# Optimization experiments

Measured on AMD Instinct MI355X. Metric: run time of the kernel, lower is better.

The kernel has to match this reference:

```python
import jax, jax.numpy as jnp
import numpy as np

B, C, L = 32, 256, 4096

def _bn(x, g, b, m, v, eps=1e-5):
    # x: [B, C, L]; eval-mode batchnorm with running stats
    inv = jax.lax.rsqrt(v + eps)
    return (x - m[None, :, None]) * (inv * g)[None, :, None] + b[None, :, None]

def _ln(x, g, b, eps=1e-6):
    # layernorm over last dim
    mu = jnp.mean(x, axis=-1, keepdims=True)
    var = jnp.mean(jnp.square(x - mu), axis=-1, keepdims=True)
    return (x - mu) * jax.lax.rsqrt(var + eps) * g + b

def _conv1d(x, w, stride=1):
    # x: [B, Cin, L], w: [Cout, Cin, K]
    return jax.lax.conv_general_dilated(
        x, w, window_strides=(stride,), padding=[(1, 1)],
        dimension_numbers=('NCW', 'OIW', 'NCW'))

def _dct2_matrix(n, dtype):
    # scipy.fftpack.dct type-II, norm=None: y[k] = 2*sum_n x[n]*cos(pi*k*(2n+1)/(2N))
    k = jnp.arange(n, dtype=dtype)[:, None]
    m = jnp.arange(n, dtype=dtype)[None, :]
    return 2.0 * jnp.cos(jnp.pi * k * (2.0 * m + 1.0) / (2.0 * n))


def setup_inputs() -> dict:
    key = jax.random.key(0)
    ks = jax.random.split(key, 12)
    s_conv = 1.0 / np.sqrt(C * 3)
    s_fc1 = 1.0 / np.sqrt(C)
    s_fc2 = 1.0 / np.sqrt(2 * C)
    return {
        'x': jax.random.normal(ks[0], (B, C, L), jnp.float32),
        'conv1_w': jax.random.normal(ks[1], (C, C, 3), jnp.float32) * s_conv,
        'bn1_g': jnp.ones((C,), jnp.float32),
        'bn1_b': jnp.zeros((C,), jnp.float32),
        'bn1_m': jax.random.normal(ks[2], (C,), jnp.float32) * 0.1,
        'bn1_v': jax.random.uniform(ks[3], (C,), jnp.float32, 0.5, 1.5),
        'conv2_w': jax.random.normal(ks[4], (C, C, 3), jnp.float32) * s_conv,
        'bn2_g': jnp.ones((C,), jnp.float32),
        'bn2_b': jnp.zeros((C,), jnp.float32),
        'bn2_m': jax.random.normal(ks[5], (C,), jnp.float32) * 0.1,
        'bn2_v': jax.random.uniform(ks[6], (C,), jnp.float32, 0.5, 1.5),
        'fc1_w': jax.random.normal(ks[7], (2 * C, C), jnp.float32) * s_fc1,
        'fc2_w': jax.random.normal(ks[8], (C, 2 * C), jnp.float32) * s_fc2,
        'ln_g': jnp.ones((C,), jnp.float32),
        'ln_b': jnp.zeros((C,), jnp.float32),
    }


def reference(x, conv1_w, bn1_g, bn1_b, bn1_m, bn1_v,
              conv2_w, bn2_g, bn2_b, bn2_m, bn2_v,
              fc1_w, fc2_w, ln_g, ln_b):
    out = _bn(_conv1d(x, conv1_w), bn1_g, bn1_b, bn1_m, bn1_v)
    out = jax.nn.relu(out)
    out = _bn(_conv1d(out, conv2_w), bn2_g, bn2_b, bn2_m, bn2_v)

    # ---- FECAM (faithful to source: DCT-II along the channel axis) ----
    xp = jnp.transpose(out, (0, 2, 1))  # [B, L, C]
    Dm = _dct2_matrix(xp.shape[-1], xp.dtype)  # [C, C]
    freq = jnp.einsum('bln,kn->blk', xp, Dm)   # DCT over channel dim
    sd = _ln(freq, ln_g, ln_b)
    h = jax.nn.relu(jnp.einsum('blc,hc->blh', sd, fc1_w))      # C -> 2C
    fw = jax.nn.sigmoid(jnp.einsum('blh,ch->blc', h, fc2_w))   # 2C -> C
    fw = _ln(fw, ln_g, ln_b)  # same LayerNorm module applied again
    out = jnp.transpose(xp * fw, (0, 2, 1))  # [B, C, L]

    # inplanes == planes, stride == 1 -> identity downsample
    return jax.nn.relu(out + x)
```

## Files before the change

kernel.cpp:

```cpp
#include <hip/hip_runtime.h>
#include <math.h>

#define BB 32
#define CC 256
#define LL 4096

typedef __attribute__((ext_vector_type(8))) short bf16x8;
typedef __attribute__((ext_vector_type(4))) float f32x4;

__device__ __forceinline__ unsigned short f2bf(float f) {
  unsigned u = __float_as_uint(f);
  u = (u + 0x7FFFu + ((u >> 16) & 1u)) >> 16;
  return (unsigned short)u;
}
__device__ __forceinline__ float bf2f(unsigned short v) {
  return __uint_as_float(((unsigned)v) << 16);
}

__global__ void init_bias(const float* __restrict__ g1, const float* __restrict__ b1,
                          const float* __restrict__ m1, const float* __restrict__ v1,
                          const float* __restrict__ g2, const float* __restrict__ b2,
                          const float* __restrict__ m2, const float* __restrict__ v2,
                          float* __restrict__ b1f, float* __restrict__ b2f) {
  int c = threadIdx.x;
  b1f[c] = b1[c] - m1[c] * g1[c] * rsqrtf(v1[c] + 1e-5f);
  b2f[c] = b2[c] - m2[c] * g2[c] * rsqrtf(v2[c] + 1e-5f);
}

__global__ void init_wsw(const float* __restrict__ w1, const float* __restrict__ g1,
                         const float* __restrict__ v1,
                         const float* __restrict__ w2, const float* __restrict__ g2,
                         const float* __restrict__ v2,
                         unsigned short* __restrict__ W1sw, unsigned short* __restrict__ W2sw) {
  int id = blockIdx.x * 256 + threadIdx.x;
  int cv = id / 196608;
  int i = id - cv * 196608;
  int kc3t = i >> 13;
  int kc = kc3t / 3, t = kc3t - 3 * kc;
  int rem = i & 8191;
  int nt = rem >> 9, L = (rem >> 3) & 63, j = i & 7;
  int co = nt * 16 + (L & 15);
  int ci = kc * 32 + ((L >> 4) << 3) + j;
  if (cv == 0) {
    float s = g1[co] * rsqrtf(v1[co] + 1e-5f);
    W1sw[i] = f2bf(w1[(co * 256 + ci) * 3 + t] * s);
  } else {
    float s = g2[co] * rsqrtf(v2[co] + 1e-5f);
    W2sw[i] = f2bf(w2[(co * 256 + ci) * 3 + t] * s);
  }
}

__global__ void init_bsw(const float* __restrict__ fc1, const float* __restrict__ fc2,
                         unsigned short* __restrict__ Bd, unsigned short* __restrict__ B1,
                         unsigned short* __restrict__ B2) {
  int id = blockIdx.x * 256 + threadIdx.x;
  if (id < 65536) {
    int i = id;
    int kc = i >> 13, nt = (i >> 9) & 15, L = (i >> 3) & 63, j = i & 7;
    int n = nt * 16 + (L & 15), k = kc * 32 + (L >> 4) * 8 + j;
    double v = 2.0 * cos(3.14159265358979323846 * (double)n * (2.0 * k + 1.0) / 512.0);
    Bd[i] = f2bf((float)v);
  } else if (id < 65536 + 131072) {
    int i = id - 65536;
    int kc = i >> 14, nt = (i >> 9) & 31, L = (i >> 3) & 63, j = i & 7;
    int n = nt * 16 + (L & 15), k = kc * 32 + (L >> 4) * 8 + j;
    B1[i] = f2bf(fc1[n * 256 + k]);
  } else {
    int i = id - 65536 - 131072;
    int kc = i >> 13, nt = (i >> 9) & 15, L = (i >> 3) & 63, j = i & 7;
    int n = nt * 16 + (L & 15), k = kc * 32 + (L >> 4) * 8 + j;
    B2[i] = f2bf(fc2[n * 512 + k]);
  }
}

__global__ __launch_bounds__(256) void transpose_x(const float* __restrict__ x,
                                                   unsigned short* __restrict__ xT) {
  __shared__ unsigned short ts[64][68];
  const int tid = threadIdx.x;
  const int b = blockIdx.z, ci0 = blockIdx.y << 6, l0 = blockIdx.x << 6;
#pragma unroll
  for (int p = 0; p < 4; ++p) {
    int cc = (p << 4) + (tid >> 4);
    int ll = (tid & 15) << 2;
    float4 v = *(const float4*)&x[((((size_t)b << 8) + ci0 + cc) << 12) + l0 + ll];
    ts[ll + 0][cc] = f2bf(v.x);
    ts[ll + 1][cc] = f2bf(v.y);
    ts[ll + 2][cc] = f2bf(v.z);
    ts[ll + 3][cc] = f2bf(v.w);
  }
  __syncthreads();
#pragma unroll
  for (int p = 0; p < 4; ++p) {
    int idx = tid + (p << 8);
    int row = idx >> 4, ch = idx & 15;
    uint2 v = *(const uint2*)&ts[row][ch << 2];
    *(uint2*)&xT[((((size_t)b << 12) + l0 + row) << 8) + ci0 + (ch << 2)] = v;
  }
}

template <bool RELU, bool FRAGOUT>
__global__ __launch_bounds__(256, 3) void conv_mfma(
    const unsigned short* __restrict__ inT, const unsigned short* __restrict__ Wsw,
    const float* __restrict__ bias, unsigned short* __restrict__ outT) {
  __shared__ char smem[51232];
  unsigned short* xs = (unsigned short*)smem;
  unsigned short* smemB = (unsigned short*)(smem + 34848);
  unsigned short* swz = (unsigned short*)smem;

  const int tid = threadIdx.x;
  const int w = tid >> 6, lane = tid & 63;
  const int g = lane >> 4, c = lane & 15;
  const int l0 = blockIdx.x << 6;
  const int b = blockIdx.y;
  const size_t rowbase = ((size_t)b << 12) + l0;

  for (int idx = tid; idx < 66 * 32; idx += 256) {
    int r = idx >> 5, ch = idx & 31;
    int gl = l0 - 1 + r;
    uint4 v = {0, 0, 0, 0};
    if (gl >= 0 && gl < LL)
      v = *(const uint4*)&inT[((((size_t)b << 12) + gl) << 8) + (ch << 3)];
    *(uint4*)&xs[r * 264 + (ch << 3)] = v;
  }

  f32x4 acc[4][4];
#pragma unroll
  for (int i = 0; i < 4; ++i)
#pragma unroll
    for (int j = 0; j < 4; ++j) acc[i][j] = (f32x4){0.f, 0.f, 0.f, 0.f};

  for (int kc = 0; kc < 8; ++kc)
#pragma unroll
    for (int t = 0; t < 3; ++t) {
      __syncthreads();
      const unsigned short* src = Wsw + ((kc * 3 + t) << 13);
#pragma unroll
      for (int p = 0; p < 4; ++p) {
        int idx = tid + (p << 8);
        *(uint4*)&smemB[idx << 3] = *(const uint4*)&src[idx << 3];
      }
      __syncthreads();
      bf16x8 af[4];
#pragma unroll
      for (int mt = 0; mt < 4; ++mt)
        af[mt] = *(const bf16x8*)&xs[(mt * 16 + c + t) * 264 + (kc << 5) + (g << 3)];
#pragma unroll
      for (int nt = 0; nt < 4; ++nt) {
        bf16x8 bfv = *(const bf16x8*)&smemB[((w << 2) + nt) * 512 + (lane << 3)];
#pragma unroll
        for (int mt = 0; mt < 4; ++mt)
          acc[mt][nt] = __builtin_amdgcn_mfma_f32_16x16x32_bf16(af[mt], bfv, acc[mt][nt], 0, 0, 0);
      }
    }
  __syncthreads();

  float pb[4];
#pragma unroll
  for (int nt = 0; nt < 4; ++nt) pb[nt] = bias[(w << 6) + nt * 16 + c];
#pragma unroll
  for (int mt = 0; mt < 4; ++mt)
#pragma unroll
    for (int r = 0; r < 4; ++r) {
      int row = mt * 16 + g * 4 + r;
#pragma unroll
      for (int nt = 0; nt < 4; ++nt) {
        float v = acc[mt][nt][r] + pb[nt];
        if (RELU) v = fmaxf(v, 0.f);
        swz[row * 264 + (w << 6) + nt * 16 + c] = f2bf(v);
      }
    }
  __syncthreads();
  if (!FRAGOUT) {
#pragma unroll
    for (int i = 0; i < 8; ++i) {
      int idx = tid + (i << 8);
      int row = idx >> 5, ch = idx & 31;
      *(uint4*)&outT[((rowbase + row) << 8) + (ch << 3)] = *(const uint4*)&swz[row * 264 + (ch << 3)];
    }
  } else {
    const int MT0 = (int)(rowbase >> 4);
#pragma unroll
    for (int i = 0; i < 8; ++i) {
      int f = tid + (i << 8);
      int mtl = f >> 9, kcl = (f >> 6) & 7, L = f & 63;
      int row = mtl * 16 + (L & 15), k0 = (kcl << 5) + ((L >> 4) << 3);
      uint4 v = *(const uint4*)&swz[row * 264 + k0];
      *(uint4*)&outT[(((size_t)(MT0 + mtl) * 8 + kcl) << 9) + L * 8] = v;
    }
  }
}

template <int STAGE>
__global__ __launch_bounds__(256, 3) void gemm_stage(
    const unsigned short* __restrict__ Ag, const unsigned short* __restrict__ Bg,
    const float* __restrict__ lng, const float* __restrict__ lnb,
    unsigned short* __restrict__ Og,
    const unsigned short* __restrict__ xpsw, const float* __restrict__ xin,
    float* __restrict__ outp) {
  __shared__ char smem[53248];
  unsigned short* smemB = (unsigned short*)smem;
  unsigned short* swz = (unsigned short*)(smem + 16384);
  float* ps1 = (float*)(smem + 51200);
  float* ps2 = (float*)(smem + 51200 + 1024);

  const int tid = threadIdx.x;
  const int w = tid >> 6;
  const int lane = tid & 63;
  const int g = lane >> 4, c = lane & 15;
  const int MT0 = blockIdx.x << 2;
  const int yh = (STAGE == 1) ? blockIdx.y : 0;
  const int KC = (STAGE == 2) ? 16 : 8;
  const int AKC = (STAGE == 2) ? 16 : 8;

  f32x4 acc[4][4];
#pragma unroll
  for (int i = 0; i < 4; ++i)
#pragma unroll
    for (int j = 0; j < 4; ++j) acc[i][j] = (f32x4){0.f, 0.f, 0.f, 0.f};

  const unsigned short* bbase = Bg + ((STAGE == 1) ? (size_t)yh * 8192 : 0);
  const size_t bstride = (STAGE == 1) ? 16384 : 8192;

  for (int kc = 0; kc < KC; ++kc) {
    bf16x8 af[4];
#pragma unroll
    for (int mt = 0; mt < 4; ++mt)
      af[mt] = *(const bf16x8*)(Ag + ((size_t)(MT0 + mt) * AKC + kc) * 512 + lane * 8);
    __syncthreads();
    const unsigned short* src = bbase + (size_t)kc * bstride;
#pragma unroll
    for (int p = 0; p < 4; ++p) {
      int idx = tid + 256 * p;
      *(uint4*)&smemB[idx * 8] = *(const uint4*)&src[idx * 8];
    }
    __syncthreads();
#pragma unroll
    for (int nt = 0; nt < 4; ++nt) {
      bf16x8 bfv = *(const bf16x8*)&smemB[(w * 4 + nt) * 512 + lane * 8];
#pragma unroll
      for (int mt = 0; mt < 4; ++mt)
        acc[mt][nt] = __builtin_amdgcn_mfma_f32_16x16x32_bf16(af[mt], bfv, acc[mt][nt], 0, 0, 0);
    }
  }

  if (STAGE == 0) {
    float pg[4], pb[4];
#pragma unroll
    for (int nt = 0; nt < 4; ++nt) {
      int col = w * 64 + nt * 16 + c;
      pg[nt] = lng[col]; pb[nt] = lnb[col];
    }
#pragma unroll
    for (int mt = 0; mt < 4; ++mt)
#pragma unroll
      for (int r = 0; r < 4; ++r) {
        float s1 = 0.f, s2 = 0.f;
#pragma unroll
        for (int nt = 0; nt < 4; ++nt) { float v = acc[mt][nt][r]; s1 += v; s2 += v * v; }
#pragma unroll
        for (int m = 1; m < 16; m <<= 1) { s1 += __shfl_xor(s1, m, 64); s2 += __shfl_xor(s2, m, 64); }
        if (c == 0) {
          ps1[w * 64 + mt * 16 + g * 4 + r] = s1;
          ps2[w * 64 + mt * 16 + g * 4 + r] = s2;
        }
      }
    __syncthreads();
#pragma unroll
    for (int mt = 0; mt < 4; ++mt)
#pragma unroll
      for (int r = 0; r < 4; ++r) {
        int row = mt * 16 + g * 4 + r;
        float s1 = ps1[row] + ps1[64 + row] + ps1[128 + row] + ps1[192 + row];
        float s2 = ps2[row] + ps2[64 + row] + ps2[128 + row] + ps2[192 + row];
        float mu = s1 * (1.f / 256.f);
        float var = s2 * (1.f / 256.f) - mu * mu;
        float inv = 1.f / sqrtf(var + 1e-6f);
#pragma unroll
        for (int nt = 0; nt < 4; ++nt) {
          float v = (acc[mt][nt][r] - mu) * inv * pg[nt] + pb[nt];
          swz[row * 264 + w * 64 + nt * 16 + c] = f2bf(v);
        }
      }
    __syncthreads();
#pragma unroll
    for (int i = 0; i < 8; ++i) {
      int f = tid + 256 * i;
      int mtl = f >> 9, kcl = (f >> 6) & 7, L = f & 63;
      int row = mtl * 16 + (L & 15), k0 = kcl * 32 + (L >> 4) * 8;
      uint4 v = *(const uint4*)&swz[row * 264 + k0];
      *(uint4*)&Og[(((size_t)(MT0 + mtl) * 8 + kcl) << 9) + L * 8] = v;
    }
  }

  if (STAGE == 1) {
#pragma unroll
    for (int mt = 0; mt < 4; ++mt)
#pragma unroll
      for (int r = 0; r < 4; ++r) {
        int row = mt * 16 + g * 4 + r;
#pragma unroll
        for (int nt = 0; nt < 4; ++nt)
          swz[row * 264 + w * 64 + nt * 16 + c] = f2bf(fmaxf(acc[mt][nt][r], 0.f));
      }
    __syncthreads();
#pragma unroll
    for (int i = 0; i < 8; ++i) {
      int f = tid + 256 * i;
      int mtl = f >> 9, kcl = (f >> 6) & 7, L = f & 63;
      int row = mtl * 16 + (L & 15), k0 = kcl * 32 + (L >> 4) * 8;
      uint4 v = *(const uint4*)&swz[row * 264 + k0];
      *(uint4*)&Og[(((size_t)(MT0 + mtl) * 16 + yh * 8 + kcl) << 9) + L * 8] = v;
    }
  }

  if (STAGE == 2) {
    float pg[4], pb[4];
#pragma unroll
    for (int nt = 0; nt < 4; ++nt) {
      int col = w * 64 + nt * 16 + c;
      pg[nt] = lng[col]; pb[nt] = lnb[col];
    }
#pragma unroll
    for (int mt = 0; mt < 4; ++mt)
#pragma unroll
      for (int nt = 0; nt < 4; ++nt)
#pragma unroll
        for (int r = 0; r < 4; ++r)
          acc[mt][nt][r] = 1.f / (1.f + expf(-acc[mt][nt][r]));
#pragma unroll
    for (int mt = 0; mt < 4; ++mt)
#pragma unroll
      for (int r = 0; r < 4; ++r) {
        float s1 = 0.f, s2 = 0.f;
#pragma unroll
        for (int nt = 0; nt < 4; ++nt) { float v = acc[mt][nt][r]; s1 += v; s2 += v * v; }
#pragma unroll
        for (int m = 1; m < 16; m <<= 1) { s1 += __shfl_xor(s1, m, 64); s2 += __shfl_xor(s2, m, 64); }
        if (c == 0) {
          ps1[w * 64 + mt * 16 + g * 4 + r] = s1;
          ps2[w * 64 + mt * 16 + g * 4 + r] = s2;
        }
      }
    __syncthreads();
    float mu_[4][4], inv_[4][4];
#pragma unroll
    for (int mt = 0; mt < 4; ++mt)
#pragma unroll
      for (int r = 0; r < 4; ++r) {
        int row = mt * 16 + g * 4 + r;
        float s1 = ps1[row] + ps1[64 + row] + ps1[128 + row] + ps1[192 + row];
        float s2 = ps2[row] + ps2[64 + row] + ps2[128 + row] + ps2[192 + row];
        float mu = s1 * (1.f / 256.f);
        float var = s2 * (1.f / 256.f) - mu * mu;
        mu_[mt][r] = mu;
        inv_[mt][r] = 1.f / sqrtf(var + 1e-6f);
      }
#pragma unroll
    for (int mt = 0; mt < 4; ++mt)
#pragma unroll
      for (int nt = 0; nt < 4; ++nt) {
        alignas(8) unsigned short tmp[4];
#pragma unroll
        for (int r = 0; r < 4; ++r)
          tmp[r] = f2bf((acc[mt][nt][r] - mu_[mt][r]) * inv_[mt][r] * pg[nt] + pb[nt]);
        int col = w * 64 + nt * 16 + c;
        *(uint2*)&swz[col * 68 + mt * 16 + g * 4] = *(const uint2*)tmp;
      }
    __syncthreads();
    const int row0 = MT0 << 4;
    const int b = row0 >> 12;
    const int l0 = row0 & 4095;
    const int li = tid & 63, cq = tid >> 6;
    for (int i = 0; i < 64; ++i) {
      int ccol = cq * 64 + i;
      float fwv = bf2f(swz[ccol * 68 + li]);
      size_t xoff = (((size_t)(MT0 + (li >> 4)) * 8 + (ccol >> 5)) << 9) +
                    (((((ccol >> 3) & 3) << 4) + (li & 15)) << 3) + (ccol & 7);
      float xpv = bf2f(xpsw[xoff]);
      size_t o = ((size_t)((b << 8) + ccol)) * LL + l0 + li;
      float ov = fmaf(xpv, fwv, xin[o]);
      outp[o] = fmaxf(ov, 0.f);
    }
  }
}

extern "C" void kernel_launch(void* const* d_in, const int* in_sizes, int n_in,
                              void* d_out, int out_size, void* d_ws, size_t ws_size,
                              hipStream_t stream) {
  const float* x    = (const float*)d_in[0];
  const float* w1   = (const float*)d_in[1];
  const float* g1   = (const float*)d_in[2];
  const float* b1   = (const float*)d_in[3];
  const float* m1   = (const float*)d_in[4];
  const float* v1   = (const float*)d_in[5];
  const float* w2   = (const float*)d_in[6];
  const float* g2   = (const float*)d_in[7];
  const float* b2   = (const float*)d_in[8];
  const float* m2   = (const float*)d_in[9];
  const float* v2   = (const float*)d_in[10];
  const float* fc1  = (const float*)d_in[11];
  const float* fc2  = (const float*)d_in[12];
  const float* lng  = (const float*)d_in[13];
  const float* lnb  = (const float*)d_in[14];
  float* out = (float*)d_out;

  float* ws = (float*)d_ws;
  float* b1f = ws;
  float* b2f = ws + 256;
  unsigned short* Bd   = (unsigned short*)(ws + 512);
  unsigned short* B1   = (unsigned short*)(ws + 33280);
  unsigned short* B2   = (unsigned short*)(ws + 98816);
  unsigned short* W1sw = (unsigned short*)(ws + 164352);
  unsigned short* W2sw = (unsigned short*)(ws + 262656);
  unsigned short* xT    = (unsigned short*)(ws + 360960);
  unsigned short* sd_sw = xT;
  unsigned short* y1T  = (unsigned short*)(ws + 17138176);
  unsigned short* h_sw = y1T;
  unsigned short* xp_sw = (unsigned short*)(ws + 50692608);

  init_bias<<<1, 256, 0, stream>>>(g1, b1, m1, v1, g2, b2, m2, v2, b1f, b2f);
  init_wsw<<<1536, 256, 0, stream>>>(w1, g1, v1, w2, g2, v2, W1sw, W2sw);
  init_bsw<<<1280, 256, 0, stream>>>(fc1, fc2, Bd, B1, B2);

  transpose_x<<<dim3(64, 4, 32), 256, 0, stream>>>(x, xT);

  conv_mfma<true, false><<<dim3(64, 32), 256, 0, stream>>>(xT, W1sw, b1f, y1T);
  conv_mfma<false, true><<<dim3(64, 32), 256, 0, stream>>>(y1T, W2sw, b2f, xp_sw);

  gemm_stage<0><<<2048, 256, 0, stream>>>(xp_sw, Bd, lng, lnb, sd_sw, nullptr, nullptr, nullptr);
  gemm_stage<1><<<dim3(2048, 2), 256, 0, stream>>>(sd_sw, B1, nullptr, nullptr, h_sw,
                                                   nullptr, nullptr, nullptr);
  gemm_stage<2><<<2048, 256, 0, stream>>>(h_sw, B2, lng, lnb, nullptr, xp_sw, x, out);
}
```

Measured before the change: 653.2 us.

## Fuse DCT, FC1, FC2 and LayerNorm stages into one kernel; conv reads weights directly

The three separate GEMM stage kernels (DCT+LN, FC1+ReLU, FC2+sigmoid+LN+residual) become one kernel. The LN output and hidden chunks stay in shared memory, and FC2 accumulates over hidden chunks of 64, so the sd and h intermediates never go to global memory. The conv kernel drops its per-step shared-memory staging of weights and the barriers around it, reading weight fragments straight from global/L2, which shrinks LDS and allows higher occupancy. The cost is repeated weight reads from global/L2 per wave and a serialized FC1→FC2 chunk loop with barriers inside the fused kernel.

Result: faster. 622.5 us (-4.7%).

```diff
diff --git a/kernel.cpp b/kernel.cpp
--- a/kernel.cpp
+++ b/kernel.cpp
@@ -99,12 +99,11 @@
 }
 
 template <bool RELU, bool FRAGOUT>
-__global__ __launch_bounds__(256, 3) void conv_mfma(
+__global__ __launch_bounds__(256, 4) void conv_mfma(
     const unsigned short* __restrict__ inT, const unsigned short* __restrict__ Wsw,
     const float* __restrict__ bias, unsigned short* __restrict__ outT) {
-  __shared__ char smem[51232];
+  __shared__ char smem[34848];
   unsigned short* xs = (unsigned short*)smem;
-  unsigned short* smemB = (unsigned short*)(smem + 34848);
   unsigned short* swz = (unsigned short*)smem;
 
   const int tid = threadIdx.x;
@@ -122,6 +121,7 @@
       v = *(const uint4*)&inT[((((size_t)b << 12) + gl) << 8) + (ch << 3)];
     *(uint4*)&xs[r * 264 + (ch << 3)] = v;
   }
+  __syncthreads();
 
   f32x4 acc[4][4];
 #pragma unroll
@@ -132,21 +132,14 @@
   for (int kc = 0; kc < 8; ++kc)
 #pragma unroll
     for (int t = 0; t < 3; ++t) {
-      __syncthreads();
       const unsigned short* src = Wsw + ((kc * 3 + t) << 13);
-#pragma unroll
-      for (int p = 0; p < 4; ++p) {
-        int idx = tid + (p << 8);
-        *(uint4*)&smemB[idx << 3] = *(const uint4*)&src[idx << 3];
-      }
-      __syncthreads();
       bf16x8 af[4];
 #pragma unroll
       for (int mt = 0; mt < 4; ++mt)
         af[mt] = *(const bf16x8*)&xs[(mt * 16 + c + t) * 264 + (kc << 5) + (g << 3)];
 #pragma unroll
       for (int nt = 0; nt < 4; ++nt) {
-        bf16x8 bfv = *(const bf16x8*)&smemB[((w << 2) + nt) * 512 + (lane << 3)];
+        bf16x8 bfv = *(const bf16x8*)&src[(((w << 2) + nt) << 9) + (lane << 3)];
 #pragma unroll
         for (int mt = 0; mt < 4; ++mt)
           acc[mt][nt] = __builtin_amdgcn_mfma_f32_16x16x32_bf16(af[mt], bfv, acc[mt][nt], 0, 0, 0);
@@ -190,78 +183,64 @@
   }
 }
 
-template <int STAGE>
-__global__ __launch_bounds__(256, 3) void gemm_stage(
-    const unsigned short* __restrict__ Ag, const unsigned short* __restrict__ Bg,
+__global__ __launch_bounds__(256, 3) void gemm_fused(
+    const unsigned short* __restrict__ xp, const unsigned short* __restrict__ Bd,
+    const unsigned short* __restrict__ B1, const unsigned short* __restrict__ B2,
     const float* __restrict__ lng, const float* __restrict__ lnb,
-    unsigned short* __restrict__ Og,
-    const unsigned short* __restrict__ xpsw, const float* __restrict__ xin,
-    float* __restrict__ outp) {
-  __shared__ char smem[53248];
-  unsigned short* smemB = (unsigned short*)smem;
-  unsigned short* swz = (unsigned short*)(smem + 16384);
-  float* ps1 = (float*)(smem + 51200);
-  float* ps2 = (float*)(smem + 51200 + 1024);
+    const float* __restrict__ xin, float* __restrict__ outp) {
+  __shared__ char smem[43008];
+  unsigned short* sdS = (unsigned short*)smem;
+  unsigned short* hS = (unsigned short*)(smem + 32768);
+  float* ps1 = (float*)(smem + 40960);
+  float* ps2 = (float*)(smem + 40960 + 1024);
+  unsigned short* swz = (unsigned short*)smem;
 
   const int tid = threadIdx.x;
   const int w = tid >> 6;
   const int lane = tid & 63;
   const int g = lane >> 4, c = lane & 15;
   const int MT0 = blockIdx.x << 2;
-  const int yh = (STAGE == 1) ? blockIdx.y : 0;
-  const int KC = (STAGE == 2) ? 16 : 8;
-  const int AKC = (STAGE == 2) ? 16 : 8;
-
-  f32x4 acc[4][4];
-#pragma unroll
-  for (int i = 0; i < 4; ++i)
-#pragma unroll
-    for (int j = 0; j < 4; ++j) acc[i][j] = (f32x4){0.f, 0.f, 0.f, 0.f};
-
-  const unsigned short* bbase = Bg + ((STAGE == 1) ? (size_t)yh * 8192 : 0);
-  const size_t bstride = (STAGE == 1) ? 16384 : 8192;
-
-  for (int kc = 0; kc < KC; ++kc) {
-    bf16x8 af[4];
-#pragma unroll
-    for (int mt = 0; mt < 4; ++mt)
-      af[mt] = *(const bf16x8*)(Ag + ((size_t)(MT0 + mt) * AKC + kc) * 512 + lane * 8);
-    __syncthreads();
-    const unsigned short* src = bbase + (size_t)kc * bstride;
-#pragma unroll
-    for (int p = 0; p < 4; ++p) {
-      int idx = tid + 256 * p;
-      *(uint4*)&smemB[idx * 8] = *(const uint4*)&src[idx * 8];
-    }
-    __syncthreads();
-#pragma unroll
-    for (int nt = 0; nt < 4; ++nt) {
-      bf16x8 bfv = *(const bf16x8*)&smemB[(w * 4 + nt) * 512 + lane * 8];
+
+  float pg[4], pb[4];
+#pragma unroll
+  for (int nt = 0; nt < 4; ++nt) {
+    int col = (w << 6) + nt * 16 + c;
+    pg[nt] = lng[col]; pb[nt] = lnb[col];
+  }
+
+  {
+    f32x4 a0[4][4];
+#pragma unroll
+    for (int i = 0; i < 4; ++i)
+#pragma unroll
+      for (int j = 0; j < 4; ++j) a0[i][j] = (f32x4){0.f, 0.f, 0.f, 0.f};
+
+    for (int kc = 0; kc < 8; ++kc) {
+      bf16x8 af[4];
 #pragma unroll
       for (int mt = 0; mt < 4; ++mt)
-        acc[mt][nt] = __builtin_amdgcn_mfma_f32_16x16x32_bf16(af[mt], bfv, acc[mt][nt], 0, 0, 0);
-    }
-  }
-
-  if (STAGE == 0) {
-    float pg[4], pb[4];
-#pragma unroll
-    for (int nt = 0; nt < 4; ++nt) {
-      int col = w * 64 + nt * 16 + c;
-      pg[nt] = lng[col]; pb[nt] = lnb[col];
-    }
+        af[mt] = *(const bf16x8*)(xp + (((size_t)(MT0 + mt) << 3) + kc) * 512 + lane * 8);
+#pragma unroll
+      for (int nt = 0; nt < 4; ++nt) {
+        bf16x8 bfv = *(const bf16x8*)(Bd + (((size_t)kc << 4) + (w << 2) + nt) * 512 + lane * 8);
+#pragma unroll
+        for (int mt = 0; mt < 4; ++mt)
+          a0[mt][nt] = __builtin_amdgcn_mfma_f32_16x16x32_bf16(af[mt], bfv, a0[mt][nt], 0, 0, 0);
+      }
+    }
+
 #pragma unroll
     for (int mt = 0; mt < 4; ++mt)
 #pragma unroll
       for (int r = 0; r < 4; ++r) {
         float s1 = 0.f, s2 = 0.f;
 #pragma unroll
-        for (int nt = 0; nt < 4; ++nt) { float v = acc[mt][nt][r]; s1 += v; s2 += v * v; }
+        for (int nt = 0; nt < 4; ++nt) { float v = a0[mt][nt][r]; s1 += v; s2 += v * v; }
 #pragma unroll
         for (int m = 1; m < 16; m <<= 1) { s1 += __shfl_xor(s1, m, 64); s2 += __shfl_xor(s2, m, 64); }
         if (c == 0) {
-          ps1[w * 64 + mt * 16 + g * 4 + r] = s1;
-          ps2[w * 64 + mt * 16 + g * 4 + r] = s2;
+          ps1[(w << 6) + mt * 16 + g * 4 + r] = s1;
+          ps2[(w << 6) + mt * 16 + g * 4 + r] = s2;
         }
       }
     __syncthreads();
@@ -277,96 +256,110 @@
         float inv = 1.f / sqrtf(var + 1e-6f);
 #pragma unroll
         for (int nt = 0; nt < 4; ++nt) {
-          float v = (acc[mt][nt][r] - mu) * inv * pg[nt] + pb[nt];
-          swz[row * 264 + w * 64 + nt * 16 + c] = f2bf(v);
+          int col = (w << 6) + nt * 16 + c;
+          float v = (a0[mt][nt][r] - mu) * inv * pg[nt] + pb[nt];
+          sdS[((mt << 3) + (col >> 5)) * 512 + (((((col >> 3) & 3) << 4) | (row & 15)) << 3) +
+              (col & 7)] = f2bf(v);
         }
       }
     __syncthreads();
-#pragma unroll
-    for (int i = 0; i < 8; ++i) {
-      int f = tid + 256 * i;
-      int mtl = f >> 9, kcl = (f >> 6) & 7, L = f & 63;
-      int row = mtl * 16 + (L & 15), k0 = kcl * 32 + (L >> 4) * 8;
-      uint4 v = *(const uint4*)&swz[row * 264 + k0];
-      *(uint4*)&Og[(((size_t)(MT0 + mtl) * 8 + kcl) << 9) + L * 8] = v;
-    }
-  }
-
-  if (STAGE == 1) {
+  }
+
+  f32x4 acc[4][4];
+#pragma unroll
+  for (int i = 0; i < 4; ++i)
+#pragma unroll
+    for (int j = 0; j < 4; ++j) acc[i][j] = (f32x4){0.f, 0.f, 0.f, 0.f};
+
+  for (int hc = 0; hc < 8; ++hc) {
+    f32x4 a1[4];
+#pragma unroll
+    for (int mt = 0; mt < 4; ++mt) a1[mt] = (f32x4){0.f, 0.f, 0.f, 0.f};
+    const unsigned short* b1p = B1 + (size_t)((hc << 2) + w) * 512 + lane * 8;
+    for (int kc = 0; kc < 8; ++kc) {
+      bf16x8 bfv = *(const bf16x8*)(b1p + (size_t)kc * 16384);
+#pragma unroll
+      for (int mt = 0; mt < 4; ++mt) {
+        bf16x8 af = *(const bf16x8*)&sdS[((mt << 3) + kc) * 512 + lane * 8];
+        a1[mt] = __builtin_amdgcn_mfma_f32_16x16x32_bf16(af, bfv, a1[mt], 0, 0, 0);
+      }
+    }
 #pragma unroll
     for (int mt = 0; mt < 4; ++mt)
 #pragma unroll
       for (int r = 0; r < 4; ++r) {
         int row = mt * 16 + g * 4 + r;
-#pragma unroll
-        for (int nt = 0; nt < 4; ++nt)
-          swz[row * 264 + w * 64 + nt * 16 + c] = f2bf(fmaxf(acc[mt][nt][r], 0.f));
+        float v = fmaxf(a1[mt][r], 0.f);
+        hS[((mt << 1) + (w >> 1)) * 512 +
+           ((((((w & 1) << 1) | (c >> 3)) << 4) | (row & 15)) << 3) + (c & 7)] = f2bf(v);
       }
     __syncthreads();
 #pragma unroll
-    for (int i = 0; i < 8; ++i) {
-      int f = tid + 256 * i;
-      int mtl = f >> 9, kcl = (f >> 6) & 7, L = f & 63;
-      int row = mtl * 16 + (L & 15), k0 = kcl * 32 + (L >> 4) * 8;
-      uint4 v = *(const uint4*)&swz[row * 264 + k0];
-      *(uint4*)&Og[(((size_t)(MT0 + mtl) * 16 + yh * 8 + kcl) << 9) + L * 8] = v;
-    }
-  }
-
-  if (STAGE == 2) {
-    float pg[4], pb[4];
+    for (int kcl = 0; kcl < 2; ++kcl) {
+      bf16x8 af2[4];
+#pragma unroll
+      for (int mt = 0; mt < 4; ++mt)
+        af2[mt] = *(const bf16x8*)&hS[((mt << 1) + kcl) * 512 + lane * 8];
+#pragma unroll
+      for (int nt = 0; nt < 4; ++nt) {
+        bf16x8 bfv = *(const bf16x8*)(B2 + (size_t)((((hc << 1) + kcl) << 4) + (w << 2) + nt) * 512 +
+                                      lane * 8);
+#pragma unroll
+        for (int mt = 0; mt < 4; ++mt)
+          acc[mt][nt] = __builtin_amdgcn_mfma_f32_16x16x32_bf16(af2[mt], bfv, acc[mt][nt], 0, 0, 0);
+      }
+    }
+    __syncthreads();
+  }
+
+#pragma unroll
+  for (int mt = 0; mt < 4; ++mt)
+#pragma unroll
+    for (int nt = 0; nt < 4; ++nt)
+#pragma unroll
+      for (int r = 0; r < 4; ++r)
+        acc[mt][nt][r] = 1.f / (1.f + expf(-acc[mt][nt][r]));
+#pragma unroll
+  for (int mt = 0; mt < 4; ++mt)
+#pragma unroll
+    for (int r = 0; r < 4; ++r) {
+      float s1 = 0.f, s2 = 0.f;
+#pragma unroll
+      for (int nt = 0; nt < 4; ++nt) { float v = acc[mt][nt][r]; s1 += v; s2 += v * v; }
+#pragma unroll
+      for (int m = 1; m < 16; m <<= 1) { s1 += __shfl_xor(s1, m, 64); s2 += __shfl_xor(s2, m, 64); }
+      if (c == 0) {
+        ps1[(w << 6) + mt * 16 + g * 4 + r] = s1;
+        ps2[(w << 6) + mt * 16 + g * 4 + r] = s2;
+      }
+    }
+  __syncthreads();
+  float mu_[4][4], inv_[4][4];
+#pragma unroll
+  for (int mt = 0; mt < 4; ++mt)
+#pragma unroll
+    for (int r = 0; r < 4; ++r) {
+      int row = mt * 16 + g * 4 + r;
+      float s1 = ps1[row] + ps1[64 + row] + ps1[128 + row] + ps1[192 + row];
+      float s2 = ps2[row] + ps2[64 + row] + ps2[128 + row] + ps2[192 + row];
+      float mu = s1 * (1.f / 256.f);
+      float var = s2 * (1.f / 256.f) - mu * mu;
+      mu_[mt][r] = mu;
+      inv_[mt][r] = 1.f / sqrtf(var + 1e-6f);
+    }
+#pragma unroll
+  for (int mt = 0; mt < 4; ++mt)
 #pragma unroll
     for (int nt = 0; nt < 4; ++nt) {
-      int col = w * 64 + nt * 16 + c;
-      pg[nt] = lng[col]; pb[nt] = lnb[col];
-    }
-#pragma unroll
-    for (int mt = 0; mt < 4; ++mt)
-#pragma unroll
-      for (int nt = 0; nt < 4; ++nt)
-#pragma unroll
-        for (int r = 0; r < 4; ++r)
-          acc[mt][nt][r] = 1.f / (1.f + expf(-acc[mt][nt][r]));
-#pragma unroll
-    for (int mt = 0; mt < 4; ++mt)
-#pragma unroll
-      for (int r = 0; r < 4; ++r) {
-        float s1 = 0.f, s2 = 0.f;
-#pragma unroll
-        for (int nt = 0; nt < 4; ++nt) { float v = acc[mt][nt][r]; s1 += v; s2 += v * v; }
-#pragma unroll
-        for (int m = 1; m < 16; m <<= 1) { s1 += __shfl_xor(s1, m, 64); s2 += __shfl_xor(s2, m, 64); }
-        if (c == 0) {
-          ps1[w * 64 + mt * 16 + g * 4 + r] = s1;
-          ps2[w * 64 + mt * 16 + g * 4 + r] = s2;
-        }
-      }
-    __syncthreads();
-    float mu_[4][4], inv_[4][4];
-#pragma unroll
-    for (int mt = 0; mt < 4; ++mt)
-#pragma unroll
-      for (int r = 0; r < 4; ++r) {
-        int row = mt * 16 + g * 4 + r;
-        float s1 = ps1[row] + ps1[64 + row] + ps1[128 + row] + ps1[192 + row];
-        float s2 = ps2[row] + ps2[64 + row] + ps2[128 + row] + ps2[192 + row];
-        float mu = s1 * (1.f / 256.f);
-        float var = s2 * (1.f / 256.f) - mu * mu;
-        mu_[mt][r] = mu;
-        inv_[mt][r] = 1.f / sqrtf(var + 1e-6f);
-      }
-#pragma unroll
-    for (int mt = 0; mt < 4; ++mt)
-#pragma unroll
-      for (int nt = 0; nt < 4; ++nt) {
-        alignas(8) unsigned short tmp[4];
-#pragma unroll
-        for (int r = 0; r < 4; ++r)
-          tmp[r] = f2bf((acc[mt][nt][r] - mu_[mt][r]) * inv_[mt][r] * pg[nt] + pb[nt]);
-        int col = w * 64 + nt * 16 + c;
-        *(uint2*)&swz[col * 68 + mt * 16 + g * 4] = *(const uint2*)tmp;
-      }
-    __syncthreads();
+      alignas(8) unsigned short tmp[4];
+#pragma unroll
+      for (int r = 0; r < 4; ++r)
+        tmp[r] = f2bf((acc[mt][nt][r] - mu_[mt][r]) * inv_[mt][r] * pg[nt] + pb[nt]);
+      int col = (w << 6) + nt * 16 + c;
+      *(uint2*)&swz[col * 68 + mt * 16 + g * 4] = *(const uint2*)tmp;
+    }
+  __syncthreads();
+  {
     const int row0 = MT0 << 4;
     const int b = row0 >> 12;
     const int l0 = row0 & 4095;
@@ -376,7 +369,7 @@
       float fwv = bf2f(swz[ccol * 68 + li]);
       size_t xoff = (((size_t)(MT0 + (li >> 4)) * 8 + (ccol >> 5)) << 9) +
                     (((((ccol >> 3) & 3) << 4) + (li & 15)) << 3) + (ccol & 7);
-      float xpv = bf2f(xpsw[xoff]);
+      float xpv = bf2f(xp[xoff]);
       size_t o = ((size_t)((b << 8) + ccol)) * LL + l0 + li;
       float ov = fmaf(xpv, fwv, xin[o]);
       outp[o] = fmaxf(ov, 0.f);
@@ -413,9 +406,7 @@
   unsigned short* W1sw = (unsigned short*)(ws + 164352);
   unsigned short* W2sw = (unsigned short*)(ws + 262656);
   unsigned short* xT    = (unsigned short*)(ws + 360960);
-  unsigned short* sd_sw = xT;
   unsigned short* y1T  = (unsigned short*)(ws + 17138176);
-  unsigned short* h_sw = y1T;
   unsigned short* xp_sw = (unsigned short*)(ws + 50692608);
 
   init_bias<<<1, 256, 0, stream>>>(g1, b1, m1, v1, g2, b2, m2, v2, b1f, b2f);
@@ -427,8 +418,5 @@
   conv_mfma<true, false><<<dim3(64, 32), 256, 0, stream>>>(xT, W1sw, b1f, y1T);
   conv_mfma<false, true><<<dim3(64, 32), 256, 0, stream>>>(y1T, W2sw, b2f, xp_sw);
 
-  gemm_stage<0><<<2048, 256, 0, stream>>>(xp_sw, Bd, lng, lnb, sd_sw, nullptr, nullptr, nullptr);
-  gemm_stage<1><<<dim3(2048, 2), 256, 0, stream>>>(sd_sw, B1, nullptr, nullptr, h_sw,
-                                                   nullptr, nullptr, nullptr);
-  gemm_stage<2><<<2048, 256, 0, stream>>>(h_sw, B2, lng, lnb, nullptr, xp_sw, x, out);
-}
+  gemm_fused<<<2048, 256, 0, stream>>>(xp_sw, Bd, B1, B2, lng, lnb, x, out);
+}
```
